# Kernel tuning notes

Hardware: AMD Instinct MI355X
Metric: run time of the kernel (lower is better)

The kernel has to match this reference:

```python
import jax, jax.numpy as jnp
import numpy as np

FILTERS = 256
B, H, W = 16, 64, 64
LN_EPS = 1e-5


def setup_inputs() -> dict:
    key = jax.random.key(0)
    ks = jax.random.split(key, 6)
    C = FILTERS
    scale = 1.0 / np.sqrt(C)  # kaiming-ish init for 1x1 convs
    return {
        "x": jax.random.normal(ks[0], (B, C, H, W), dtype=jnp.float32),
        "g": jax.random.normal(ks[1], (B, C, H, W), dtype=jnp.float32),
        "Wx": jax.random.normal(ks[2], (C, C), dtype=jnp.float32) * scale,
        "Wg": jax.random.normal(ks[3], (C, C), dtype=jnp.float32) * scale,
        "Wpsi": jax.random.normal(ks[4], (1, C), dtype=jnp.float32) * scale,
        "ln_gamma": jnp.ones((C,), dtype=jnp.float32),
        "ln_beta": jnp.zeros((C,), dtype=jnp.float32),
        "bxg": jnp.zeros((C,), dtype=jnp.float32),
        "bpsi": jnp.zeros((1,), dtype=jnp.float32),
    }


def reference(x, g, Wx, Wg, Wpsi, ln_gamma, ln_beta, bxg, bpsi):
    # 1x1 convs == per-pixel channel GEMMs: [B,C,H,W] x [O,C] -> [B,O,H,W]
    x_conv = jnp.einsum("bchw,oc->bohw", x, Wx)
    g_conv = jnp.einsum("bchw,oc->bohw", g, Wg)
    att = jax.nn.relu(x_conv + g_conv + bxg[None, :, None, None])
    # LayerNorm over channel dim (original permutes to NHWC, LN over last dim)
    mean = jnp.mean(att, axis=1, keepdims=True)
    var = jnp.mean(jnp.square(att - mean), axis=1, keepdims=True)
    att = (att - mean) * jax.lax.rsqrt(var + LN_EPS)
    att = att * ln_gamma[None, :, None, None] + ln_beta[None, :, None, None]
    # psi: 1x1 conv to single channel + bias, sigmoid gate
    att = jnp.einsum("bchw,oc->bohw", att, Wpsi) + bpsi[None, :, None, None]
    att = jax.nn.sigmoid(att)  # [B,1,H,W]
    return att * x
```

## Files before the change

kernel.cpp:

```cpp
#include <hip/hip_runtime.h>
#include <stdint.h>


typedef __bf16 bf16x8 __attribute__((ext_vector_type(8)));
typedef float f32x4 __attribute__((ext_vector_type(4)));

#define STR 40
#define LN_EPS 1e-5f

__device__ __forceinline__ uint16_t f2b(float f) {
    union { float f; uint32_t i; } v; v.f = f;
    uint32_t x = v.i;
    return (uint16_t)((x + 0x7FFFu + ((x >> 16) & 1u)) >> 16);
}

struct EpiShared {
    float red[3][4][64];
    float psi[64];
    float cpart[8];
};

union ALds {
    uint16_t a[2][2][64 * STR];
    EpiShared e;
};

__global__ void wconv_kernel(const float* __restrict__ Wx, const float* __restrict__ Wg,
                             uint16_t* __restrict__ ox, uint16_t* __restrict__ og) {
    const int i  = blockIdx.x * 256 + threadIdx.x;
    const int n  = i >> 6;
    const int k4 = (i & 63) * 4;
    const int it = k4 >> 5;
    const int kk = k4 & 31;
    const int dst = it * 8192 + n * 32 + kk;
    const float4 a = *(const float4*)&Wx[n * 256 + k4];
    const float4 b = *(const float4*)&Wg[n * 256 + k4];
    uint2 pa, pb;
    pa.x = (uint32_t)f2b(a.x) | ((uint32_t)f2b(a.y) << 16);
    pa.y = (uint32_t)f2b(a.z) | ((uint32_t)f2b(a.w) << 16);
    pb.x = (uint32_t)f2b(b.x) | ((uint32_t)f2b(b.y) << 16);
    pb.y = (uint32_t)f2b(b.z) | ((uint32_t)f2b(b.w) << 16);
    *(uint2*)&ox[dst] = pa;
    *(uint2*)&og[dst] = pb;
}

__device__ __forceinline__ void stage_load(float av[16], const float* __restrict__ Asrc,
                                           size_t abase, int c0, int px) {
    #pragma unroll
    for (int j = 0; j < 2; ++j)
        #pragma unroll
        for (int c = 0; c < 8; ++c)
            av[j * 8 + c] = Asrc[abase + (size_t)(c0 + j * 16 + c) * 4096 + px];
}

__device__ __forceinline__ void stage_store(const float av[16], uint16_t* dstrow, int c0) {
    #pragma unroll
    for (int j = 0; j < 2; ++j) {
        uint4 w;
        w.x = (uint32_t)f2b(av[j*8+0]) | ((uint32_t)f2b(av[j*8+1]) << 16);
        w.y = (uint32_t)f2b(av[j*8+2]) | ((uint32_t)f2b(av[j*8+3]) << 16);
        w.z = (uint32_t)f2b(av[j*8+4]) | ((uint32_t)f2b(av[j*8+5]) << 16);
        w.w = (uint32_t)f2b(av[j*8+6]) | ((uint32_t)f2b(av[j*8+7]) << 16);
        *(uint4*)&dstrow[c0 + j * 16] = w;
    }
}

__global__ __launch_bounds__(256, 3) void attgate_kernel(
    const float* __restrict__ x,
    const float* __restrict__ g,
    const uint16_t* __restrict__ Wxb,
    const uint16_t* __restrict__ Wgb,
    const float* __restrict__ Wpsi,
    const float* __restrict__ gamma,
    const float* __restrict__ beta,
    const float* __restrict__ bxg,
    const float* __restrict__ bpsi,
    float* __restrict__ out)
{
    __shared__ __align__(16) ALds u;

    const int t    = threadIdx.x;
    const int lane = t & 63;
    const int wv   = t >> 6;
    const int ln   = lane & 15;
    const int q    = lane >> 4;

    const int gp0  = blockIdx.x * 64;
    const int b    = gp0 >> 12;
    const int pix0 = gp0 & 4095;
    const size_t xbase = (size_t)b * (256 * 4096) + pix0;

    f32x4 acc[4][4];
    #pragma unroll
    for (int i = 0; i < 4; ++i)
        #pragma unroll
        for (int j = 0; j < 4; ++j)
            acc[i][j] = (f32x4){0.f, 0.f, 0.f, 0.f};

    const int at  = t & 127;
    const int px  = at & 63;
    const int cg  = at >> 6;
    const int c0  = cg * 8;
    const float* Asrc = (t < 128) ? x : g;
    const int tens    = (t < 128) ? 0 : 1;

    float av[16];
    stage_load(av, Asrc, xbase, c0, px);
    stage_store(av, &u.a[0][tens][px * STR], c0);

    const int fro = wv * 64 + ln;

    for (int it = 0; it < 8; ++it) {
        __syncthreads();
        const int cur = it & 1;
        const uint16_t* Wxi = Wxb + it * 8192;
        const uint16_t* Wgi = Wgb + it * 8192;

        bf16x8 bx[4];
        #pragma unroll
        for (int nt = 0; nt < 4; ++nt)
            bx[nt] = *(const bf16x8*)&Wxi[(fro + nt * 16) * 32 + q * 8];

        if (it < 7)
            stage_load(av, Asrc, xbase + (size_t)((it + 1) * 32) * 4096, c0, px);

        bf16x8 af[4];
        #pragma unroll
        for (int mt = 0; mt < 4; ++mt)
            af[mt] = *(const bf16x8*)&u.a[cur][0][(mt * 16 + ln) * STR + q * 8];
        #pragma unroll
        for (int mt = 0; mt < 4; ++mt)
            #pragma unroll
            for (int nt = 0; nt < 4; ++nt)
                acc[mt][nt] = __builtin_amdgcn_mfma_f32_16x16x32_bf16(af[mt], bx[nt], acc[mt][nt], 0, 0, 0);

        bf16x8 bg[4];
        #pragma unroll
        for (int nt = 0; nt < 4; ++nt)
            bg[nt] = *(const bf16x8*)&Wgi[(fro + nt * 16) * 32 + q * 8];
        #pragma unroll
        for (int mt = 0; mt < 4; ++mt)
            af[mt] = *(const bf16x8*)&u.a[cur][1][(mt * 16 + ln) * STR + q * 8];
        #pragma unroll
        for (int mt = 0; mt < 4; ++mt)
            #pragma unroll
            for (int nt = 0; nt < 4; ++nt)
                acc[mt][nt] = __builtin_amdgcn_mfma_f32_16x16x32_bf16(af[mt], bg[nt], acc[mt][nt], 0, 0, 0);

        if (it < 7)
            stage_store(av, &u.a[cur ^ 1][tens][px * STR], c0);
    }

    __syncthreads();

    {
        float a  = Wpsi[t] * gamma[t];
        float bb = Wpsi[t] * beta[t];
        #pragma unroll
        for (int off = 32; off; off >>= 1) {
            a  += __shfl_xor(a, off, 64);
            bb += __shfl_xor(bb, off, 64);
        }
        if (lane == 0) { u.e.cpart[wv] = a; u.e.cpart[4 + wv] = bb; }
    }

    float biasv[4], Ac[4];
    #pragma unroll
    for (int nt = 0; nt < 4; ++nt) {
        const int o = wv * 64 + nt * 16 + ln;
        biasv[nt] = bxg[o];
        Ac[nt]    = Wpsi[o] * gamma[o];
    }
    __syncthreads();
    const float sumA = u.e.cpart[0] + u.e.cpart[1] + u.e.cpart[2] + u.e.cpart[3];
    const float sumB = u.e.cpart[4] + u.e.cpart[5] + u.e.cpart[6] + u.e.cpart[7];

    #pragma unroll
    for (int mt = 0; mt < 4; ++mt) {
        #pragma unroll
        for (int r = 0; r < 4; ++r) {
            float s = 0.f, ss = 0.f, tt = 0.f;
            #pragma unroll
            for (int nt = 0; nt < 4; ++nt) {
                float v = acc[mt][nt][r] + biasv[nt];
                v = fmaxf(v, 0.f);
                s += v; ss += v * v; tt += Ac[nt] * v;
            }
            #pragma unroll
            for (int off = 1; off < 16; off <<= 1) {
                s  += __shfl_xor(s,  off, 64);
                ss += __shfl_xor(ss, off, 64);
                tt += __shfl_xor(tt, off, 64);
            }
            if (ln == 0) {
                const int pix = mt * 16 + q * 4 + r;
                u.e.red[0][wv][pix] = s;
                u.e.red[1][wv][pix] = ss;
                u.e.red[2][wv][pix] = tt;
            }
        }
    }
    __syncthreads();

    if (t < 64) {
        const float s  = u.e.red[0][0][t] + u.e.red[0][1][t] + u.e.red[0][2][t] + u.e.red[0][3][t];
        const float ss = u.e.red[1][0][t] + u.e.red[1][1][t] + u.e.red[1][2][t] + u.e.red[1][3][t];
        const float tt = u.e.red[2][0][t] + u.e.red[2][1][t] + u.e.red[2][2][t] + u.e.red[2][3][t];
        const float mu   = s * (1.f / 256.f);
        const float var  = ss * (1.f / 256.f) - mu * mu;
        const float rstd = rsqrtf(var + LN_EPS);
        const float z    = rstd * (tt - mu * sumA) + sumB + bpsi[0];
        u.e.psi[t] = 1.f / (1.f + __expf(-z));
    }
    __syncthreads();

    const int pc = (t & 15) * 4;
    const float p0 = u.e.psi[pc], p1 = u.e.psi[pc + 1], p2 = u.e.psi[pc + 2], p3 = u.e.psi[pc + 3];
    const int crow = t >> 4;
    #pragma unroll
    for (int pass = 0; pass < 16; ++pass) {
        const int c = pass * 16 + crow;
        const size_t off = xbase + (size_t)c * 4096 + pc;
        const float4 d = *(const float4*)&x[off];
        float4 o;
        o.x = d.x * p0; o.y = d.y * p1; o.z = d.z * p2; o.w = d.w * p3;
        *(float4*)&out[off] = o;
    }
}

extern "C" void kernel_launch(void* const* d_in, const int* in_sizes, int n_in,
                              void* d_out, int out_size, void* d_ws, size_t ws_size,
                              hipStream_t stream) {
    const float* x    = (const float*)d_in[0];
    const float* g    = (const float*)d_in[1];
    const float* Wx   = (const float*)d_in[2];
    const float* Wg   = (const float*)d_in[3];
    const float* Wpsi = (const float*)d_in[4];
    const float* gam  = (const float*)d_in[5];
    const float* bet  = (const float*)d_in[6];
    const float* bxg  = (const float*)d_in[7];
    const float* bpsi = (const float*)d_in[8];
    float* out        = (float*)d_out;

    uint16_t* Wxb = (uint16_t*)d_ws;
    uint16_t* Wgb = (uint16_t*)((char*)d_ws + 131072);

    wconv_kernel<<<dim3(64), dim3(256), 0, stream>>>(Wx, Wg, Wxb, Wgb);
    attgate_kernel<<<dim3(1024), dim3(256), 0, stream>>>(
        x, g, Wxb, Wgb, Wpsi, gam, bet, bxg, bpsi, out);
}
```

Before: 205.6 us.

## Halve pixel tile per block to 32 and double-buffer loads with register ping-pong

```diff
diff --git a/kernel.cpp b/kernel.cpp
--- a/kernel.cpp
+++ b/kernel.cpp
@@ -15,13 +15,13 @@
 }
 
 struct EpiShared {
-    float red[3][4][64];
-    float psi[64];
+    float red[3][4][32];
+    float psi[32];
     float cpart[8];
 };
 
 union ALds {
-    uint16_t a[2][2][64 * STR];
+    uint16_t a[2][2][32 * STR];
     EpiShared e;
 };
 
@@ -44,28 +44,23 @@
     *(uint2*)&og[dst] = pb;
 }
 
-__device__ __forceinline__ void stage_load(float av[16], const float* __restrict__ Asrc,
+__device__ __forceinline__ void stage_load(float av[8], const float* __restrict__ Asrc,
                                            size_t abase, int c0, int px) {
     #pragma unroll
-    for (int j = 0; j < 2; ++j)
-        #pragma unroll
-        for (int c = 0; c < 8; ++c)
-            av[j * 8 + c] = Asrc[abase + (size_t)(c0 + j * 16 + c) * 4096 + px];
-}
-
-__device__ __forceinline__ void stage_store(const float av[16], uint16_t* dstrow, int c0) {
-    #pragma unroll
-    for (int j = 0; j < 2; ++j) {
-        uint4 w;
-        w.x = (uint32_t)f2b(av[j*8+0]) | ((uint32_t)f2b(av[j*8+1]) << 16);
-        w.y = (uint32_t)f2b(av[j*8+2]) | ((uint32_t)f2b(av[j*8+3]) << 16);
-        w.z = (uint32_t)f2b(av[j*8+4]) | ((uint32_t)f2b(av[j*8+5]) << 16);
-        w.w = (uint32_t)f2b(av[j*8+6]) | ((uint32_t)f2b(av[j*8+7]) << 16);
-        *(uint4*)&dstrow[c0 + j * 16] = w;
-    }
-}
-
-__global__ __launch_bounds__(256, 3) void attgate_kernel(
+    for (int c = 0; c < 8; ++c)
+        av[c] = Asrc[abase + (size_t)(c0 + c) * 4096 + px];
+}
+
+__device__ __forceinline__ void stage_store(const float av[8], uint16_t* dst) {
+    uint4 w;
+    w.x = (uint32_t)f2b(av[0]) | ((uint32_t)f2b(av[1]) << 16);
+    w.y = (uint32_t)f2b(av[2]) | ((uint32_t)f2b(av[3]) << 16);
+    w.z = (uint32_t)f2b(av[4]) | ((uint32_t)f2b(av[5]) << 16);
+    w.w = (uint32_t)f2b(av[6]) | ((uint32_t)f2b(av[7]) << 16);
+    *(uint4*)dst = w;
+}
+
+__global__ __launch_bounds__(256, 6) void attgate_kernel(
     const float* __restrict__ x,
     const float* __restrict__ g,
     const uint16_t* __restrict__ Wxb,
@@ -85,70 +80,111 @@
     const int ln   = lane & 15;
     const int q    = lane >> 4;
 
-    const int gp0  = blockIdx.x * 64;
+    const int gp0  = blockIdx.x * 32;
     const int b    = gp0 >> 12;
     const int pix0 = gp0 & 4095;
     const size_t xbase = (size_t)b * (256 * 4096) + pix0;
 
-    f32x4 acc[4][4];
-    #pragma unroll
-    for (int i = 0; i < 4; ++i)
+    f32x4 acc[2][4];
+    #pragma unroll
+    for (int i = 0; i < 2; ++i)
         #pragma unroll
         for (int j = 0; j < 4; ++j)
             acc[i][j] = (f32x4){0.f, 0.f, 0.f, 0.f};
 
     const int at  = t & 127;
-    const int px  = at & 63;
-    const int cg  = at >> 6;
-    const int c0  = cg * 8;
+    const int px  = at & 31;
+    const int c0  = (at >> 5) * 8;
     const float* Asrc = (t < 128) ? x : g;
     const int tens    = (t < 128) ? 0 : 1;
-
-    float av[16];
-    stage_load(av, Asrc, xbase, c0, px);
-    stage_store(av, &u.a[0][tens][px * STR], c0);
+    uint16_t* dst0 = &u.a[0][tens][px * STR + c0];
+    uint16_t* dst1 = &u.a[1][tens][px * STR + c0];
+    const size_t abase = xbase + (size_t)c0 * 4096 + px;
 
     const int fro = wv * 64 + ln;
 
-    for (int it = 0; it < 8; ++it) {
+    float avA[8], avB[8];
+    stage_load(avA, Asrc, abase, 0, 0);
+    stage_store(avA, dst0);
+    stage_load(avA, Asrc, abase + (size_t)32 * 4096, 0, 0);
+
+    #pragma unroll 1
+    for (int it = 0; it < 8; it += 2) {
         __syncthreads();
-        const int cur = it & 1;
-        const uint16_t* Wxi = Wxb + it * 8192;
-        const uint16_t* Wgi = Wgb + it * 8192;
-
-        bf16x8 bx[4];
-        #pragma unroll
-        for (int nt = 0; nt < 4; ++nt)
-            bx[nt] = *(const bf16x8*)&Wxi[(fro + nt * 16) * 32 + q * 8];
-
-        if (it < 7)
-            stage_load(av, Asrc, xbase + (size_t)((it + 1) * 32) * 4096, c0, px);
-
-        bf16x8 af[4];
-        #pragma unroll
-        for (int mt = 0; mt < 4; ++mt)
-            af[mt] = *(const bf16x8*)&u.a[cur][0][(mt * 16 + ln) * STR + q * 8];
-        #pragma unroll
-        for (int mt = 0; mt < 4; ++mt)
-            #pragma unroll
-            for (int nt = 0; nt < 4; ++nt)
-                acc[mt][nt] = __builtin_amdgcn_mfma_f32_16x16x32_bf16(af[mt], bx[nt], acc[mt][nt], 0, 0, 0);
-
-        bf16x8 bg[4];
-        #pragma unroll
-        for (int nt = 0; nt < 4; ++nt)
-            bg[nt] = *(const bf16x8*)&Wgi[(fro + nt * 16) * 32 + q * 8];
-        #pragma unroll
-        for (int mt = 0; mt < 4; ++mt)
-            af[mt] = *(const bf16x8*)&u.a[cur][1][(mt * 16 + ln) * STR + q * 8];
-        #pragma unroll
-        for (int mt = 0; mt < 4; ++mt)
-            #pragma unroll
-            for (int nt = 0; nt < 4; ++nt)
-                acc[mt][nt] = __builtin_amdgcn_mfma_f32_16x16x32_bf16(af[mt], bg[nt], acc[mt][nt], 0, 0, 0);
-
-        if (it < 7)
-            stage_store(av, &u.a[cur ^ 1][tens][px * STR], c0);
+        {
+            const uint16_t* Wxi = Wxb + it * 8192;
+            const uint16_t* Wgi = Wgb + it * 8192;
+            bf16x8 bx[4];
+            #pragma unroll
+            for (int nt = 0; nt < 4; ++nt)
+                bx[nt] = *(const bf16x8*)&Wxi[(fro + nt * 16) * 32 + q * 8];
+
+            if (it + 2 < 8)
+                stage_load(avB, Asrc, abase + (size_t)((it + 2) * 32) * 4096, 0, 0);
+
+            bf16x8 af[2];
+            #pragma unroll
+            for (int mt = 0; mt < 2; ++mt)
+                af[mt] = *(const bf16x8*)&u.a[0][0][(mt * 16 + ln) * STR + q * 8];
+            #pragma unroll
+            for (int mt = 0; mt < 2; ++mt)
+                #pragma unroll
+                for (int nt = 0; nt < 4; ++nt)
+                    acc[mt][nt] = __builtin_amdgcn_mfma_f32_16x16x32_bf16(af[mt], bx[nt], acc[mt][nt], 0, 0, 0);
+
+            bf16x8 bg[4];
+            #pragma unroll
+            for (int nt = 0; nt < 4; ++nt)
+                bg[nt] = *(const bf16x8*)&Wgi[(fro + nt * 16) * 32 + q * 8];
+            #pragma unroll
+            for (int mt = 0; mt < 2; ++mt)
+                af[mt] = *(const bf16x8*)&u.a[0][1][(mt * 16 + ln) * STR + q * 8];
+            #pragma unroll
+            for (int mt = 0; mt < 2; ++mt)
+                #pragma unroll
+                for (int nt = 0; nt < 4; ++nt)
+                    acc[mt][nt] = __builtin_amdgcn_mfma_f32_16x16x32_bf16(af[mt], bg[nt], acc[mt][nt], 0, 0, 0);
+
+            stage_store(avA, dst1);
+        }
+        __syncthreads();
+        {
+            const uint16_t* Wxi = Wxb + (it + 1) * 8192;
+            const uint16_t* Wgi = Wgb + (it + 1) * 8192;
+            bf16x8 bx[4];
+            #pragma unroll
+            for (int nt = 0; nt < 4; ++nt)
+                bx[nt] = *(const bf16x8*)&Wxi[(fro + nt * 16) * 32 + q * 8];
+
+            if (it + 3 < 8)
+                stage_load(avA, Asrc, abase + (size_t)((it + 3) * 32) * 4096, 0, 0);
+
+            bf16x8 af[2];
+            #pragma unroll
+            for (int mt = 0; mt < 2; ++mt)
+                af[mt] = *(const bf16x8*)&u.a[1][0][(mt * 16 + ln) * STR + q * 8];
+            #pragma unroll
+            for (int mt = 0; mt < 2; ++mt)
+                #pragma unroll
+                for (int nt = 0; nt < 4; ++nt)
+                    acc[mt][nt] = __builtin_amdgcn_mfma_f32_16x16x32_bf16(af[mt], bx[nt], acc[mt][nt], 0, 0, 0);
+
+            bf16x8 bg[4];
+            #pragma unroll
+            for (int nt = 0; nt < 4; ++nt)
+                bg[nt] = *(const bf16x8*)&Wgi[(fro + nt * 16) * 32 + q * 8];
+            #pragma unroll
+            for (int mt = 0; mt < 2; ++mt)
+                af[mt] = *(const bf16x8*)&u.a[1][1][(mt * 16 + ln) * STR + q * 8];
+            #pragma unroll
+            for (int mt = 0; mt < 2; ++mt)
+                #pragma unroll
+                for (int nt = 0; nt < 4; ++nt)
+                    acc[mt][nt] = __builtin_amdgcn_mfma_f32_16x16x32_bf16(af[mt], bg[nt], acc[mt][nt], 0, 0, 0);
+
+            if (it + 2 < 8)
+                stage_store(avB, dst0);
+        }
     }
 
     __syncthreads();
@@ -176,7 +212,7 @@
     const float sumB = u.e.cpart[4] + u.e.cpart[5] + u.e.cpart[6] + u.e.cpart[7];
 
     #pragma unroll
-    for (int mt = 0; mt < 4; ++mt) {
+    for (int mt = 0; mt < 2; ++mt) {
         #pragma unroll
         for (int r = 0; r < 4; ++r) {
             float s = 0.f, ss = 0.f, tt = 0.f;
@@ -202,7 +238,7 @@
     }
     __syncthreads();
 
-    if (t < 64) {
+    if (t < 32) {
         const float s  = u.e.red[0][0][t] + u.e.red[0][1][t] + u.e.red[0][2][t] + u.e.red[0][3][t];
         const float ss = u.e.red[1][0][t] + u.e.red[1][1][t] + u.e.red[1][2][t] + u.e.red[1][3][t];
         const float tt = u.e.red[2][0][t] + u.e.red[2][1][t] + u.e.red[2][2][t] + u.e.red[2][3][t];
@@ -214,12 +250,12 @@
     }
     __syncthreads();
 
-    const int pc = (t & 15) * 4;
+    const int pc = (t & 7) * 4;
     const float p0 = u.e.psi[pc], p1 = u.e.psi[pc + 1], p2 = u.e.psi[pc + 2], p3 = u.e.psi[pc + 3];
-    const int crow = t >> 4;
-    #pragma unroll
-    for (int pass = 0; pass < 16; ++pass) {
-        const int c = pass * 16 + crow;
+    const int crow = t >> 3;
+    #pragma unroll
+    for (int pass = 0; pass < 8; ++pass) {
+        const int c = pass * 32 + crow;
         const size_t off = xbase + (size_t)c * 4096 + pc;
         const float4 d = *(const float4*)&x[off];
         float4 o;
@@ -246,6 +282,6 @@
     uint16_t* Wgb = (uint16_t*)((char*)d_ws + 131072);
 
     wconv_kernel<<<dim3(64), dim3(256), 0, stream>>>(Wx, Wg, Wxb, Wgb);
-    attgate_kernel<<<dim3(1024), dim3(256), 0, stream>>>(
+    attgate_kernel<<<dim3(2048), dim3(256), 0, stream>>>(
         x, g, Wxb, Wgb, Wpsi, gam, bet, bxg, bpsi, out);
 }
```

New measurement: 292.1 us. +42.1%, slower.
